# Kernel tuning notes

Hardware: AMD Instinct MI355X
Metric: run time of the kernel (lower is better)

The kernel has to match this reference:

```python
import jax, jax.numpy as jnp
import numpy as np

B, T, D, E, FF, K = 4, 1024, 1024, 8, 2048, 2
SINKHORN_ITERS = 3


def setup_inputs() -> dict:
    key = jax.random.key(0)
    ks = jax.random.split(key, 7)
    scale = 0.02
    return {
        "x": jax.random.normal(ks[0], (B, T, D), dtype=jnp.float32),
        "router_w": jax.random.normal(ks[1], (E, D), dtype=jnp.float32) * scale,  # nn.Linear(D,E).weight
        "router_b": jnp.zeros((E,), dtype=jnp.float32),
        "temperature": jnp.ones((1,), dtype=jnp.float32) * 0.5,
        "wg": jax.random.normal(ks[2], (E, D, FF), dtype=jnp.float32) * scale,   # expert gate weights
        "wp": jax.random.normal(ks[3], (E, D, FF), dtype=jnp.float32) * scale,   # expert proj weights
        "wo": jax.random.normal(ks[4], (E, FF, D), dtype=jnp.float32) * scale,   # expert out_proj weights
    }


def _sinkhorn(log_alpha, iters=SINKHORN_ITERS):
    for _ in range(iters):
        log_alpha = log_alpha - jax.nn.logsumexp(log_alpha, axis=-1, keepdims=True)
        log_alpha = log_alpha - jax.nn.logsumexp(log_alpha, axis=-2, keepdims=True)
    gates = jnp.exp(log_alpha)
    return gates / (jnp.sum(gates, axis=-1, keepdims=True) + 1e-8)


def reference(x, router_w, router_b, temperature, wg, wp, wo):
    # Router scores with clamped temperature (clamp(min=0.1))
    temp = jnp.maximum(temperature, 0.1)
    scores = (jnp.einsum("btd,ed->bte", x, router_w) + router_b) / temp  # [B,T,E]

    # T>1 and E>1 -> Sinkhorn doubly-stochastic normalization
    gates = _sinkhorn(scores)

    topk_vals, topk_idx = jax.lax.top_k(gates, K)                 # [B,T,K]
    topk_gates = topk_vals / (jnp.sum(topk_vals, axis=-1, keepdims=True) + 1e-8)

    # Dense all-expert FFN (relu-gated GLU), matching mask-and-sum semantics.
    # sum_k sum_i (idx_k==i)*gate_k*expert_i(x) == sum_k gate_k * expert_{idx_k}(x)
    g = jax.nn.relu(jnp.einsum("btd,edf->btef", x, wg))           # [B,T,E,FF]
    p = jnp.einsum("btd,edf->btef", x, wp)                        # [B,T,E,FF]
    all_out = jnp.einsum("btef,efd->bted", g * p, wo)             # [B,T,E,D]

    gathered = jnp.take_along_axis(all_out, topk_idx[..., None], axis=2)  # [B,T,K,D]
    expert_out = jnp.sum(gathered * topk_gates[..., None], axis=2)        # [B,T,D]

    return x + expert_out
```

## Files before the change

kernel.cpp:

```cpp
#include <hip/hip_runtime.h>
#include <hip/hip_bf16.h>
#include <stdint.h>

#define B_   4
#define T_   1024
#define D_   1024
#define E_   8
#define FF_  2048
#define NT_  4096
#define LCAP 9216
#define NT1  (D_ / 32)
#define NT2  (FF_ / 32)

typedef unsigned short u16;
typedef __attribute__((ext_vector_type(8))) short bf16x8;
typedef __attribute__((ext_vector_type(4))) float f32x4;

#define MFMA16(a, b, c) __builtin_amdgcn_mfma_f32_16x16x32_bf16((a), (b), (c), 0, 0, 0)

__device__ __forceinline__ u16 f2bf(float f) {
  union { float f; uint32_t u; } c; c.f = f;
  return (u16)((c.u + 0x7FFFu + ((c.u >> 16) & 1u)) >> 16);
}

__device__ __forceinline__ void gl_lds16(const void* g, void* l) {
  __builtin_amdgcn_global_load_lds(
      (const __attribute__((address_space(1))) uint32_t*)g,
      (__attribute__((address_space(3))) uint32_t*)l, 16, 0, 0);
}


__global__ __launch_bounds__(256) void k_init(int* __restrict__ tok, float* __restrict__ gate,
                                              int* __restrict__ cnt, int* __restrict__ cur) {
  int i = blockIdx.x * 256 + threadIdx.x;
  if (i < LCAP) { tok[i] = 0; gate[i] = 0.f; }
  if (i < E_)   { cnt[i] = 0; cur[i] = 0; }
}

__global__ __launch_bounds__(256) void k_prep(const float4* __restrict__ x4,
                                              float4* __restrict__ out4,
                                              ushort4* __restrict__ xb4) {
  int i = blockIdx.x * 256 + threadIdx.x;
  float4 v = x4[i];
  out4[i] = v;
  ushort4 o; o.x = f2bf(v.x); o.y = f2bf(v.y); o.z = f2bf(v.z); o.w = f2bf(v.w);
  xb4[i] = o;
}

__global__ __launch_bounds__(256) void k_router(const float* __restrict__ x,
                                                const float* __restrict__ rw,
                                                const float* __restrict__ rb,
                                                const float* __restrict__ temp,
                                                float* __restrict__ scores) {
  int wid  = (blockIdx.x * 256 + threadIdx.x) >> 6;
  int lane = threadIdx.x & 63;
  const float* xr = x + (size_t)wid * D_;
  float acc[E_];
  #pragma unroll
  for (int e = 0; e < E_; ++e) acc[e] = 0.f;
  for (int i = lane; i < D_; i += 64) {
    float xv = xr[i];
    #pragma unroll
    for (int e = 0; e < E_; ++e) acc[e] += xv * rw[e * D_ + i];
  }
  float inv = 1.0f / fmaxf(temp[0], 0.1f);
  #pragma unroll
  for (int e = 0; e < E_; ++e) {
    float v = acc[e];
    for (int off = 32; off; off >>= 1) v += __shfl_xor(v, off);
    if (lane == 0) scores[(size_t)wid * E_ + e] = (v + rb[e]) * inv;
  }
}

__global__ __launch_bounds__(1024) void k_sinkhorn(const float* __restrict__ scores,
                                                   float* __restrict__ tkg, int* __restrict__ tki,
                                                   int* __restrict__ cnt) {
  const int b = blockIdx.x, t = threadIdx.x;
  const int row = b * T_ + t;
  float s[E_];
  #pragma unroll
  for (int e = 0; e < E_; ++e) s[e] = scores[(size_t)row * E_ + e];

  __shared__ float red[16][E_];
  __shared__ int lcnt[E_];
  if (t < E_) lcnt[t] = 0;
  const int wid = t >> 6, lane = t & 63;

  for (int it = 0; it < 3; ++it) {
    float m = s[0];
    #pragma unroll
    for (int e = 1; e < E_; ++e) m = fmaxf(m, s[e]);
    float sum = 0.f;
    #pragma unroll
    for (int e = 0; e < E_; ++e) sum += expf(s[e] - m);
    float lse = m + logf(sum);
    #pragma unroll
    for (int e = 0; e < E_; ++e) s[e] -= lse;

    float cm[E_];
    #pragma unroll
    for (int e = 0; e < E_; ++e) {
      float v = s[e];
      for (int off = 32; off; off >>= 1) v = fmaxf(v, __shfl_xor(v, off));
      if (lane == 0) red[wid][e] = v;
    }
    __syncthreads();
    #pragma unroll
    for (int e = 0; e < E_; ++e) {
      float mm = red[0][e];
      for (int wv = 1; wv < 16; ++wv) mm = fmaxf(mm, red[wv][e]);
      cm[e] = mm;
    }
    __syncthreads();
    #pragma unroll
    for (int e = 0; e < E_; ++e) {
      float v = expf(s[e] - cm[e]);
      for (int off = 32; off; off >>= 1) v += __shfl_xor(v, off);
      if (lane == 0) red[wid][e] = v;
    }
    __syncthreads();
    #pragma unroll
    for (int e = 0; e < E_; ++e) {
      float ss = 0.f;
      for (int wv = 0; wv < 16; ++wv) ss += red[wv][e];
      s[e] -= cm[e] + logf(ss);
    }
    __syncthreads();
  }

  float g[E_]; float rs = 0.f;
  #pragma unroll
  for (int e = 0; e < E_; ++e) { g[e] = expf(s[e]); rs += g[e]; }
  float inv = 1.f / (rs + 1e-8f);
  #pragma unroll
  for (int e = 0; e < E_; ++e) g[e] *= inv;

  int i0 = 0; float v0 = g[0];
  #pragma unroll
  for (int e = 1; e < E_; ++e) if (g[e] > v0) { v0 = g[e]; i0 = e; }
  int i1 = -1; float v1 = -1e30f;
  #pragma unroll
  for (int e = 0; e < E_; ++e) if (e != i0 && g[e] > v1) { v1 = g[e]; i1 = e; }
  float den = 1.f / (v0 + v1 + 1e-8f);
  tkg[row * 2 + 0] = v0 * den; tki[row * 2 + 0] = i0;
  tkg[row * 2 + 1] = v1 * den; tki[row * 2 + 1] = i1;

  atomicAdd(&lcnt[i0], 1);
  atomicAdd(&lcnt[i1], 1);
  __syncthreads();
  if (t < E_) atomicAdd(&cnt[t], lcnt[t]);
}

__global__ void k_offsets(const int* __restrict__ cnt, int* __restrict__ segoff) {
  if (threadIdx.x == 0 && blockIdx.x == 0) {
    int run = 0;
    for (int e = 0; e < E_; ++e) { segoff[e] = run; run += ((cnt[e] + 127) >> 7) << 7; }
  }
}

__global__ __launch_bounds__(256) void k_scatter(const int* __restrict__ tki, const float* __restrict__ tkg,
                                                 const int* __restrict__ segoff, int* __restrict__ cur,
                                                 int* __restrict__ tok, float* __restrict__ gate) {
  int idx = blockIdx.x * 256 + threadIdx.x;
  int row = idx >> 1;
  int e = tki[idx];
  float g = tkg[idx];
  int pos = atomicAdd(&cur[e], 1);
  int p = segoff[e] + pos;
  tok[p] = row;
  gate[p] = g;
}

__global__ __launch_bounds__(256) void k_transpose(const float* __restrict__ in, u16* __restrict__ out,
                                                   int R, int C) {
  __shared__ __align__(16) u16 t[32][36];
  const size_t msz = (size_t)R * C;
  const float* A = in + blockIdx.z * msz;
  u16* O = out + blockIdx.z * msz;
  const int r0 = blockIdx.y * 32, c0 = blockIdx.x * 32;
  const int tid = threadIdx.x;
  {
    const int i = tid >> 3, j4 = (tid & 7) << 2;
    const float4 v = *(const float4*)(A + (size_t)(r0 + i) * C + c0 + j4);
    ushort4 pk; pk.x = f2bf(v.x); pk.y = f2bf(v.y); pk.z = f2bf(v.z); pk.w = f2bf(v.w);
    *(ushort4*)(&t[i][j4]) = pk;
  }
  __syncthreads();
  {
    const int j2 = tid & 15;
    #pragma unroll
    for (int it = 0; it < 2; ++it) {
      const int r = (tid >> 4) + it * 16;
      uint32_t pv = (uint32_t)t[2 * j2][r] | ((uint32_t)t[2 * j2 + 1][r] << 16);
      *(uint32_t*)(O + (size_t)(c0 + r) * R + r0 + 2 * j2) = pv;
    }
  }
}


__global__ __launch_bounds__(512, 4) void k_stage1(
    const u16* __restrict__ wgT, const u16* __restrict__ wpT,
    const u16* __restrict__ xb, const int* __restrict__ tok,
    const int* __restrict__ cnt, const int* __restrict__ segoff,
    u16* __restrict__ H) {
  const int raw = blockIdx.x;
  const int e   = raw & 7;
  const int rem = raw >> 3;
  const int ft  = rem >> 5;
  const int pt  = rem & 31;
  if (pt * 128 >= cnt[e]) return;
  const int tid = threadIdx.x;
  const int lane = tid & 63;
  const int w = tid >> 6;
  const int lane15 = lane & 15, lchunk = lane >> 4;
  const int fw = w >> 2, pw = w & 3;

  __shared__ __align__(16) u16 LG[3][4096];
  __shared__ __align__(16) u16 LP[3][4096];
  __shared__ __align__(16) u16 LX[3][4096];

  const int prow0 = segoff[e] + pt * 128;
  const size_t wb = (size_t)e * FF_ * D_ + (size_t)(ft * 128 + w * 16 + lane15) * D_ + lchunk * 8;
  const u16* gsrc = wgT + wb;
  const u16* psrc = wpT + wb;
  const int tk = tok[prow0 + w * 16 + lane15];
  const u16* xsrc = xb + (size_t)tk * D_ + lchunk * 8;
  const int dstb = w * 512;

  const f32x4 vz = {0.f, 0.f, 0.f, 0.f};
  f32x4 accG[4][2], accP[4][2];
  #pragma unroll
  for (int m = 0; m < 4; ++m)
    #pragma unroll
    for (int n = 0; n < 2; ++n) { accG[m][n] = vz; accP[m][n] = vz; }

#define ISSUE1(c, t) do { const int o_ = (t) * 32;                 \
    gl_lds16(gsrc + o_, &LG[c][dstb]);                             \
    gl_lds16(psrc + o_, &LP[c][dstb]);                             \
    gl_lds16(xsrc + o_, &LX[c][dstb]); } while (0)

#define COMP1(c) do {                                                        \
    const u16* lg = LG[c]; const u16* lp = LP[c]; const u16* lx = LX[c];     \
    bf16x8 ag[4], ap[4], bx[2];                                              \
    _Pragma("unroll")                                                        \
    for (int m = 0; m < 4; ++m) {                                            \
      ag[m] = *(const bf16x8*)(lg + (fw * 4 + m) * 512 + lane * 8);          \
      ap[m] = *(const bf16x8*)(lp + (fw * 4 + m) * 512 + lane * 8);          \
    }                                                                        \
    _Pragma("unroll")                                                        \
    for (int n = 0; n < 2; ++n)                                              \
      bx[n] = *(const bf16x8*)(lx + (pw * 2 + n) * 512 + lane * 8);          \
    __builtin_amdgcn_s_setprio(1);                                           \
    _Pragma("unroll")                                                        \
    for (int m = 0; m < 4; ++m)                                              \
      _Pragma("unroll")                                                      \
      for (int n = 0; n < 2; ++n) {                                          \
        accG[m][n] = MFMA16(ag[m], bx[n], accG[m][n]);                       \
        accP[m][n] = MFMA16(ap[m], bx[n], accP[m][n]);                       \
      }                                                                      \
    __builtin_amdgcn_s_setprio(0); } while (0)

  ISSUE1(0, 0);
  ISSUE1(1, 1);
  #pragma unroll 1
  for (int t = 0; t < NT1 - 1; ++t) {
    asm volatile("s_waitcnt vmcnt(3)" ::: "memory");
    __builtin_amdgcn_s_barrier();
    asm volatile("" ::: "memory");
    if (t + 2 < NT1) { const int cn = (t + 2) % 3; ISSUE1(cn, t + 2); }
    const int c = t % 3;
    COMP1(c);
  }
  asm volatile("s_waitcnt vmcnt(0)" ::: "memory");
  __builtin_amdgcn_s_barrier();
  asm volatile("" ::: "memory");
  COMP1((NT1 - 1) % 3);
#undef ISSUE1
#undef COMP1

  const int jrow = lchunk * 4;
  #pragma unroll
  for (int m = 0; m < 4; ++m) {
    #pragma unroll
    for (int n = 0; n < 2; ++n) {
      union { uint2 v; u16 s[4]; } u;
      #pragma unroll
      for (int j = 0; j < 4; ++j)
        u.s[j] = f2bf(fmaxf(accG[m][n][j], 0.f) * accP[m][n][j]);
      const int prow = prow0 + pw * 32 + n * 16 + lane15;
      const int fcol = ft * 128 + fw * 64 + m * 16 + jrow;
      *(uint2*)(H + (size_t)prow * FF_ + fcol) = u.v;
    }
  }
}

__global__ __launch_bounds__(512, 4) void k_stage2(
    const u16* __restrict__ H, const u16* __restrict__ woT,
    const int* __restrict__ tok, const float* __restrict__ gate,
    const int* __restrict__ cnt, const int* __restrict__ segoff,
    float* __restrict__ out) {
  const int raw = blockIdx.x;
  const int e   = raw & 7;
  const int rem = raw >> 3;
  const int dt  = rem >> 5;
  const int pt  = rem & 31;
  if (pt * 128 >= cnt[e]) return;
  const int tid = threadIdx.x;
  const int lane = tid & 63;
  const int w = tid >> 6;
  const int lane15 = lane & 15, lchunk = lane >> 4;
  const int ph = w >> 2, dq = w & 3;

  __shared__ __align__(16) u16 LH[3][4096];
  __shared__ __align__(16) u16 LW[3][8192];
  __shared__ int   ltok[128];
  __shared__ float lgt[128];

  const int prow0 = segoff[e] + pt * 128;
  if (tid < 128) { ltok[tid] = tok[prow0 + tid]; lgt[tid] = gate[prow0 + tid]; }

  const u16* hsrc  = H + (size_t)(prow0 + w * 16 + lane15) * FF_ + lchunk * 8;
  const u16* wsrc0 = woT + (size_t)e * D_ * FF_ + (size_t)(dt * 256 + w * 16 + lane15) * FF_ + lchunk * 8;
  const u16* wsrc1 = wsrc0 + (size_t)128 * FF_;
  const int dstb = w * 512;

  const f32x4 vz = {0.f, 0.f, 0.f, 0.f};
  f32x4 acc[4][4];
  #pragma unroll
  for (int m = 0; m < 4; ++m)
    #pragma unroll
    for (int n = 0; n < 4; ++n) acc[m][n] = vz;

#define ISSUE2(c, t) do { const int o_ = (t) * 32;                 \
    gl_lds16(hsrc + o_,  &LH[c][dstb]);                            \
    gl_lds16(wsrc0 + o_, &LW[c][dstb]);                            \
    gl_lds16(wsrc1 + o_, &LW[c][dstb + 4096]); } while (0)

#define COMP2(c) do {                                                        \
    const u16* lh = LH[c]; const u16* lw = LW[c];                            \
    bf16x8 ah[4], bw[4];                                                     \
    _Pragma("unroll")                                                        \
    for (int m = 0; m < 4; ++m)                                              \
      ah[m] = *(const bf16x8*)(lh + (ph * 4 + m) * 512 + lane * 8);          \
    _Pragma("unroll")                                                        \
    for (int n = 0; n < 4; ++n)                                              \
      bw[n] = *(const bf16x8*)(lw + (dq * 4 + n) * 512 + lane * 8);          \
    __builtin_amdgcn_s_setprio(1);                                           \
    _Pragma("unroll")                                                        \
    for (int m = 0; m < 4; ++m)                                              \
      _Pragma("unroll")                                                      \
      for (int n = 0; n < 4; ++n)                                            \
        acc[m][n] = MFMA16(ah[m], bw[n], acc[m][n]);                         \
    __builtin_amdgcn_s_setprio(0); } while (0)

  ISSUE2(0, 0);
  ISSUE2(1, 1);
  #pragma unroll 1
  for (int t = 0; t < NT2 - 1; ++t) {
    asm volatile("s_waitcnt vmcnt(3)" ::: "memory");
    __builtin_amdgcn_s_barrier();
    asm volatile("" ::: "memory");
    if (t + 2 < NT2) { const int cn = (t + 2) % 3; ISSUE2(cn, t + 2); }
    const int c = t % 3;
    COMP2(c);
  }
  asm volatile("s_waitcnt vmcnt(0)" ::: "memory");
  __builtin_amdgcn_s_barrier();
  asm volatile("" ::: "memory");
  COMP2((NT2 - 1) % 3);
#undef ISSUE2
#undef COMP2

  const int jrow = lchunk * 4;
  #pragma unroll
  for (int m = 0; m < 4; ++m) {
    #pragma unroll
    for (int n = 0; n < 4; ++n) {
      const int dcol = dt * 256 + dq * 64 + n * 16 + lane15;
      #pragma unroll
      for (int j = 0; j < 4; ++j) {
        const int pl = ph * 64 + m * 16 + jrow + j;
        unsafeAtomicAdd(&out[(size_t)ltok[pl] * D_ + dcol], lgt[pl] * acc[m][n][j]);
      }
    }
  }
}


extern "C" void kernel_launch(void* const* d_in, const int* in_sizes, int n_in,
                              void* d_out, int out_size, void* d_ws, size_t ws_size,
                              hipStream_t stream) {
  const float* x    = (const float*)d_in[0];
  const float* rw   = (const float*)d_in[1];
  const float* rb   = (const float*)d_in[2];
  const float* temp = (const float*)d_in[3];
  const float* wg   = (const float*)d_in[4];
  const float* wp   = (const float*)d_in[5];
  const float* wo   = (const float*)d_in[6];
  float* out = (float*)d_out;
  char* ws = (char*)d_ws;

  const size_t O_XB  = 0;
  const size_t O_WGT = 8388608;
  const size_t O_WPT = O_WGT + 33554432;
  const size_t O_WOT = O_WGT;
  const size_t O_H   = O_WPT + 33554432;
  const size_t O_SC  = O_H + (size_t)LCAP * FF_ * 2;
  const size_t O_TKG = O_SC + (size_t)NT_ * E_ * 4;
  const size_t O_TKI = O_TKG + (size_t)NT_ * 2 * 4;
  const size_t O_CNT = O_TKI + (size_t)NT_ * 2 * 4;
  const size_t O_CUR = O_CNT + 128;
  const size_t O_SEG = O_CUR + 128;
  const size_t O_TOK = O_SEG + 128;
  const size_t O_GTE = O_TOK + (size_t)LCAP * 4;
  const size_t REQ   = O_GTE + (size_t)LCAP * 4;
  if (ws_size < REQ) return;

  u16*   xb     = (u16*)(ws + O_XB);
  u16*   wgT    = (u16*)(ws + O_WGT);
  u16*   wpT    = (u16*)(ws + O_WPT);
  u16*   woT    = (u16*)(ws + O_WOT);
  u16*   Hbuf   = (u16*)(ws + O_H);
  float* scores = (float*)(ws + O_SC);
  float* tkg    = (float*)(ws + O_TKG);
  int*   tki    = (int*)(ws + O_TKI);
  int*   cnt    = (int*)(ws + O_CNT);
  int*   cur    = (int*)(ws + O_CUR);
  int*   segoff = (int*)(ws + O_SEG);
  int*   tok    = (int*)(ws + O_TOK);
  float* gate   = (float*)(ws + O_GTE);

  k_init<<<(LCAP + 255) / 256, 256, 0, stream>>>(tok, gate, cnt, cur);
  k_prep<<<(NT_ * D_ / 4) / 256, 256, 0, stream>>>((const float4*)x, (float4*)out, (ushort4*)xb);
  k_router<<<NT_ / 4, 256, 0, stream>>>(x, rw, rb, temp, scores);
  k_sinkhorn<<<B_, 1024, 0, stream>>>(scores, tkg, tki, cnt);
  k_offsets<<<1, 64, 0, stream>>>(cnt, segoff);
  k_scatter<<<(NT_ * 2) / 256, 256, 0, stream>>>(tki, tkg, segoff, cur, tok, gate);

  k_transpose<<<dim3(FF_ / 32, D_ / 32, E_), 256, 0, stream>>>(wg, wgT, D_, FF_);
  k_transpose<<<dim3(FF_ / 32, D_ / 32, E_), 256, 0, stream>>>(wp, wpT, D_, FF_);

  k_stage1<<<32 * 16 * E_, 512, 0, stream>>>(wgT, wpT, xb, tok, cnt, segoff, Hbuf);

  k_transpose<<<dim3(D_ / 32, FF_ / 32, E_), 256, 0, stream>>>(wo, woT, FF_, D_);

  k_stage2<<<32 * 4 * E_, 512, 0, stream>>>(Hbuf, woT, tok, gate, cnt, segoff, out);
}
```

Baseline: 473.8 us.

## Fuse prep into router and retile expert GEMMs to 256-thread blocks

Removes the separate prep kernel by having the router write the residual copy and the bf16 copy of x while it reads x. Both expert GEMM kernels move from 512 to 256 threads per block. Each wave now owns a larger accumulator tile (stage1 goes to 4x4 per gate/proj, stage2 uses a 128-wide D tile with twice the grid). The aim is more reuse per LDS fragment load and better MFMA density. The cost is higher register pressure and lower wave occupancy, and the router's stores are scalar 2-byte writes instead of vectorized ones.

Result: no change. 479.7 us (+1.2%).

```diff
diff --git a/kernel.cpp b/kernel.cpp
--- a/kernel.cpp
+++ b/kernel.cpp
@@ -37,29 +37,25 @@
   if (i < E_)   { cnt[i] = 0; cur[i] = 0; }
 }
 
-__global__ __launch_bounds__(256) void k_prep(const float4* __restrict__ x4,
-                                              float4* __restrict__ out4,
-                                              ushort4* __restrict__ xb4) {
-  int i = blockIdx.x * 256 + threadIdx.x;
-  float4 v = x4[i];
-  out4[i] = v;
-  ushort4 o; o.x = f2bf(v.x); o.y = f2bf(v.y); o.z = f2bf(v.z); o.w = f2bf(v.w);
-  xb4[i] = o;
-}
-
 __global__ __launch_bounds__(256) void k_router(const float* __restrict__ x,
                                                 const float* __restrict__ rw,
                                                 const float* __restrict__ rb,
                                                 const float* __restrict__ temp,
-                                                float* __restrict__ scores) {
+                                                float* __restrict__ scores,
+                                                float* __restrict__ out,
+                                                u16* __restrict__ xb) {
   int wid  = (blockIdx.x * 256 + threadIdx.x) >> 6;
   int lane = threadIdx.x & 63;
   const float* xr = x + (size_t)wid * D_;
+  float* orow = out + (size_t)wid * D_;
+  u16* xrow = xb + (size_t)wid * D_;
   float acc[E_];
   #pragma unroll
   for (int e = 0; e < E_; ++e) acc[e] = 0.f;
   for (int i = lane; i < D_; i += 64) {
     float xv = xr[i];
+    orow[i] = xv;
+    xrow[i] = f2bf(xv);
     #pragma unroll
     for (int e = 0; e < E_; ++e) acc[e] += xv * rw[e * D_ + i];
   }
@@ -198,7 +194,7 @@
 }
 
 
-__global__ __launch_bounds__(512, 4) void k_stage1(
+__global__ __launch_bounds__(256, 2) void k_stage1(
     const u16* __restrict__ wgT, const u16* __restrict__ wpT,
     const u16* __restrict__ xb, const int* __restrict__ tok,
     const int* __restrict__ cnt, const int* __restrict__ segoff,
@@ -213,48 +209,54 @@
   const int lane = tid & 63;
   const int w = tid >> 6;
   const int lane15 = lane & 15, lchunk = lane >> 4;
-  const int fw = w >> 2, pw = w & 3;
+  const int fw = w >> 1, pw = w & 1;
 
   __shared__ __align__(16) u16 LG[3][4096];
   __shared__ __align__(16) u16 LP[3][4096];
   __shared__ __align__(16) u16 LX[3][4096];
 
   const int prow0 = segoff[e] + pt * 128;
-  const size_t wb = (size_t)e * FF_ * D_ + (size_t)(ft * 128 + w * 16 + lane15) * D_ + lchunk * 8;
-  const u16* gsrc = wgT + wb;
-  const u16* psrc = wpT + wb;
-  const int tk = tok[prow0 + w * 16 + lane15];
-  const u16* xsrc = xb + (size_t)tk * D_ + lchunk * 8;
-  const int dstb = w * 512;
+  const size_t wb0 = (size_t)e * FF_ * D_ + (size_t)(ft * 128 + w * 16 + lane15) * D_ + lchunk * 8;
+  const size_t wb1 = wb0 + (size_t)64 * D_;
+  const u16* gsrc0 = wgT + wb0;  const u16* gsrc1 = wgT + wb1;
+  const u16* psrc0 = wpT + wb0;  const u16* psrc1 = wpT + wb1;
+  const int tk0 = tok[prow0 + w * 16 + lane15];
+  const int tk1 = tok[prow0 + 64 + w * 16 + lane15];
+  const u16* xsrc0 = xb + (size_t)tk0 * D_ + lchunk * 8;
+  const u16* xsrc1 = xb + (size_t)tk1 * D_ + lchunk * 8;
+  const int dst0 = w * 512, dst1 = (w + 4) * 512;
 
   const f32x4 vz = {0.f, 0.f, 0.f, 0.f};
-  f32x4 accG[4][2], accP[4][2];
+  f32x4 accG[4][4], accP[4][4];
   #pragma unroll
   for (int m = 0; m < 4; ++m)
     #pragma unroll
-    for (int n = 0; n < 2; ++n) { accG[m][n] = vz; accP[m][n] = vz; }
+    for (int n = 0; n < 4; ++n) { accG[m][n] = vz; accP[m][n] = vz; }
 
 #define ISSUE1(c, t) do { const int o_ = (t) * 32;                 \
-    gl_lds16(gsrc + o_, &LG[c][dstb]);                             \
-    gl_lds16(psrc + o_, &LP[c][dstb]);                             \
-    gl_lds16(xsrc + o_, &LX[c][dstb]); } while (0)
+    gl_lds16(gsrc0 + o_, &LG[c][dst0]);                            \
+    gl_lds16(gsrc1 + o_, &LG[c][dst1]);                            \
+    gl_lds16(psrc0 + o_, &LP[c][dst0]);                            \
+    gl_lds16(psrc1 + o_, &LP[c][dst1]);                            \
+    gl_lds16(xsrc0 + o_, &LX[c][dst0]);                            \
+    gl_lds16(xsrc1 + o_, &LX[c][dst1]); } while (0)
 
 #define COMP1(c) do {                                                        \
     const u16* lg = LG[c]; const u16* lp = LP[c]; const u16* lx = LX[c];     \
-    bf16x8 ag[4], ap[4], bx[2];                                              \
+    bf16x8 ag[4], ap[4], bx[4];                                              \
     _Pragma("unroll")                                                        \
     for (int m = 0; m < 4; ++m) {                                            \
       ag[m] = *(const bf16x8*)(lg + (fw * 4 + m) * 512 + lane * 8);          \
       ap[m] = *(const bf16x8*)(lp + (fw * 4 + m) * 512 + lane * 8);          \
     }                                                                        \
     _Pragma("unroll")                                                        \
-    for (int n = 0; n < 2; ++n)                                              \
-      bx[n] = *(const bf16x8*)(lx + (pw * 2 + n) * 512 + lane * 8);          \
+    for (int n = 0; n < 4; ++n)                                              \
+      bx[n] = *(const bf16x8*)(lx + (pw * 4 + n) * 512 + lane * 8);          \
     __builtin_amdgcn_s_setprio(1);                                           \
     _Pragma("unroll")                                                        \
     for (int m = 0; m < 4; ++m)                                              \
       _Pragma("unroll")                                                      \
-      for (int n = 0; n < 2; ++n) {                                          \
+      for (int n = 0; n < 4; ++n) {                                          \
         accG[m][n] = MFMA16(ag[m], bx[n], accG[m][n]);                       \
         accP[m][n] = MFMA16(ap[m], bx[n], accP[m][n]);                       \
       }                                                                      \
@@ -264,7 +266,7 @@
   ISSUE1(1, 1);
   #pragma unroll 1
   for (int t = 0; t < NT1 - 1; ++t) {
-    asm volatile("s_waitcnt vmcnt(3)" ::: "memory");
+    asm volatile("s_waitcnt vmcnt(6)" ::: "memory");
     __builtin_amdgcn_s_barrier();
     asm volatile("" ::: "memory");
     if (t + 2 < NT1) { const int cn = (t + 2) % 3; ISSUE1(cn, t + 2); }
@@ -282,19 +284,19 @@
   #pragma unroll
   for (int m = 0; m < 4; ++m) {
     #pragma unroll
-    for (int n = 0; n < 2; ++n) {
+    for (int n = 0; n < 4; ++n) {
       union { uint2 v; u16 s[4]; } u;
       #pragma unroll
       for (int j = 0; j < 4; ++j)
         u.s[j] = f2bf(fmaxf(accG[m][n][j], 0.f) * accP[m][n][j]);
-      const int prow = prow0 + pw * 32 + n * 16 + lane15;
+      const int prow = prow0 + pw * 64 + n * 16 + lane15;
       const int fcol = ft * 128 + fw * 64 + m * 16 + jrow;
       *(uint2*)(H + (size_t)prow * FF_ + fcol) = u.v;
     }
   }
 }
 
-__global__ __launch_bounds__(512, 4) void k_stage2(
+__global__ __launch_bounds__(256, 3) void k_stage2(
     const u16* __restrict__ H, const u16* __restrict__ woT,
     const int* __restrict__ tok, const float* __restrict__ gate,
     const int* __restrict__ cnt, const int* __restrict__ segoff,
@@ -309,20 +311,22 @@
   const int lane = tid & 63;
   const int w = tid >> 6;
   const int lane15 = lane & 15, lchunk = lane >> 4;
-  const int ph = w >> 2, dq = w & 3;
+  const int ph = w >> 1, dh = w & 1;
 
   __shared__ __align__(16) u16 LH[3][4096];
-  __shared__ __align__(16) u16 LW[3][8192];
+  __shared__ __align__(16) u16 LW[3][4096];
   __shared__ int   ltok[128];
   __shared__ float lgt[128];
 
   const int prow0 = segoff[e] + pt * 128;
   if (tid < 128) { ltok[tid] = tok[prow0 + tid]; lgt[tid] = gate[prow0 + tid]; }
 
-  const u16* hsrc  = H + (size_t)(prow0 + w * 16 + lane15) * FF_ + lchunk * 8;
-  const u16* wsrc0 = woT + (size_t)e * D_ * FF_ + (size_t)(dt * 256 + w * 16 + lane15) * FF_ + lchunk * 8;
-  const u16* wsrc1 = wsrc0 + (size_t)128 * FF_;
-  const int dstb = w * 512;
+  const u16* hsrc0 = H + (size_t)(prow0 + w * 16 + lane15) * FF_ + lchunk * 8;
+  const u16* hsrc1 = hsrc0 + (size_t)64 * FF_;
+  const u16* wsrc0 = woT + (size_t)e * D_ * FF_
+                         + (size_t)(dt * 128 + w * 16 + lane15) * FF_ + lchunk * 8;
+  const u16* wsrc1 = wsrc0 + (size_t)64 * FF_;
+  const int dst0 = w * 512, dst1 = (w + 4) * 512;
 
   const f32x4 vz = {0.f, 0.f, 0.f, 0.f};
   f32x4 acc[4][4];
@@ -332,9 +336,10 @@
     for (int n = 0; n < 4; ++n) acc[m][n] = vz;
 
 #define ISSUE2(c, t) do { const int o_ = (t) * 32;                 \
-    gl_lds16(hsrc + o_,  &LH[c][dstb]);                            \
-    gl_lds16(wsrc0 + o_, &LW[c][dstb]);                            \
-    gl_lds16(wsrc1 + o_, &LW[c][dstb + 4096]); } while (0)
+    gl_lds16(hsrc0 + o_, &LH[c][dst0]);                            \
+    gl_lds16(hsrc1 + o_, &LH[c][dst1]);                            \
+    gl_lds16(wsrc0 + o_, &LW[c][dst0]);                            \
+    gl_lds16(wsrc1 + o_, &LW[c][dst1]); } while (0)
 
 #define COMP2(c) do {                                                        \
     const u16* lh = LH[c]; const u16* lw = LW[c];                            \
@@ -344,7 +349,7 @@
       ah[m] = *(const bf16x8*)(lh + (ph * 4 + m) * 512 + lane * 8);          \
     _Pragma("unroll")                                                        \
     for (int n = 0; n < 4; ++n)                                              \
-      bw[n] = *(const bf16x8*)(lw + (dq * 4 + n) * 512 + lane * 8);          \
+      bw[n] = *(const bf16x8*)(lw + (dh * 4 + n) * 512 + lane * 8);          \
     __builtin_amdgcn_s_setprio(1);                                           \
     _Pragma("unroll")                                                        \
     for (int m = 0; m < 4; ++m)                                              \
@@ -357,7 +362,7 @@
   ISSUE2(1, 1);
   #pragma unroll 1
   for (int t = 0; t < NT2 - 1; ++t) {
-    asm volatile("s_waitcnt vmcnt(3)" ::: "memory");
+    asm volatile("s_waitcnt vmcnt(4)" ::: "memory");
     __builtin_amdgcn_s_barrier();
     asm volatile("" ::: "memory");
     if (t + 2 < NT2) { const int cn = (t + 2) % 3; ISSUE2(cn, t + 2); }
@@ -376,7 +381,7 @@
   for (int m = 0; m < 4; ++m) {
     #pragma unroll
     for (int n = 0; n < 4; ++n) {
-      const int dcol = dt * 256 + dq * 64 + n * 16 + lane15;
+      const int dcol = dt * 128 + dh * 64 + n * 16 + lane15;
       #pragma unroll
       for (int j = 0; j < 4; ++j) {
         const int pl = ph * 64 + m * 16 + jrow + j;
@@ -431,8 +436,7 @@
   float* gate   = (float*)(ws + O_GTE);
 
   k_init<<<(LCAP + 255) / 256, 256, 0, stream>>>(tok, gate, cnt, cur);
-  k_prep<<<(NT_ * D_ / 4) / 256, 256, 0, stream>>>((const float4*)x, (float4*)out, (ushort4*)xb);
-  k_router<<<NT_ / 4, 256, 0, stream>>>(x, rw, rb, temp, scores);
+  k_router<<<NT_ / 4, 256, 0, stream>>>(x, rw, rb, temp, scores, out, xb);
   k_sinkhorn<<<B_, 1024, 0, stream>>>(scores, tkg, tki, cnt);
   k_offsets<<<1, 64, 0, stream>>>(cnt, segoff);
   k_scatter<<<(NT_ * 2) / 256, 256, 0, stream>>>(tki, tkg, segoff, cur, tok, gate);
@@ -440,9 +444,9 @@
   k_transpose<<<dim3(FF_ / 32, D_ / 32, E_), 256, 0, stream>>>(wg, wgT, D_, FF_);
   k_transpose<<<dim3(FF_ / 32, D_ / 32, E_), 256, 0, stream>>>(wp, wpT, D_, FF_);
 
-  k_stage1<<<32 * 16 * E_, 512, 0, stream>>>(wgT, wpT, xb, tok, cnt, segoff, Hbuf);
+  k_stage1<<<32 * 16 * E_, 256, 0, stream>>>(wgT, wpT, xb, tok, cnt, segoff, Hbuf);
 
   k_transpose<<<dim3(D_ / 32, FF_ / 32, E_), 256, 0, stream>>>(wo, woT, FF_, D_);
 
-  k_stage2<<<32 * 4 * E_, 512, 0, stream>>>(Hbuf, woT, tok, gate, cnt, segoff, out);
-}
+  k_stage2<<<32 * 8 * E_, 256, 0, stream>>>(Hbuf, woT, tok, gate, cnt, segoff, out);
+}
```
